# Kernel optimization log

Hardware: AMD Instinct MI355X
Metric: run time of the kernel (lower is better)

Reference implementation:

```python
import jax, jax.numpy as jnp
import numpy as np

B, N, DIM = 4, 2048, 1024
HEADS, DHEAD = 16, 64
INNER = HEADS * DHEAD  # 1024


def _sigma(t):
    # elu(x) + 1 feature map (strictly positive)
    return jax.nn.elu(t) + 1.0


def setup_inputs() -> dict:
    key = jax.random.key(0)
    k1, k2, k3, k4, k5 = jax.random.split(key, 5)
    x = jax.random.normal(k1, (B, N, DIM), dtype=jnp.float32)
    M = jax.random.normal(k2, (B, HEADS, DHEAD, DHEAD), dtype=jnp.float32)
    Z = jnp.ones((B, HEADS, DHEAD, 1), dtype=jnp.float32)
    W_qkv = jax.random.normal(k3, (DIM, 3 * INNER), dtype=jnp.float32) * (DIM ** -0.5)
    beta_lin = jnp.ones((1,), dtype=jnp.float32) * 4.6     # Linear_Attention.beta
    beta_gate = jax.random.normal(k4, (1, HEADS, 1, 1), dtype=jnp.float32)  # per-head gate
    return {"x": x, "M": M, "Z": Z, "W_qkv": W_qkv, "beta_lin": beta_lin, "beta_gate": beta_gate}


def reference(x, M, Z, W_qkv, beta_lin, beta_gate):
    b, n, _ = x.shape
    scale = DHEAD ** -0.5

    qkv = x @ W_qkv                                   # [b, n, 3*inner]
    q, k, v = jnp.split(qkv, 3, axis=-1)
    # b n (h d) -> b h n d
    to_heads = lambda t: t.reshape(b, n, HEADS, DHEAD).transpose(0, 2, 1, 3)
    q, k, v = to_heads(q), to_heads(k), to_heads(v)

    # ---- linear-attention compressive memory branch ----
    sq = _sigma(q)                                    # [b h n d]
    sk = _sigma(k)
    A_mem = jnp.einsum('bhnd,bhdv->bhnv', sq, M) / jnp.einsum('bhnd,bhdi->bhni', sq, Z)
    moment = jnp.einsum('bhnd,bhdv->bhnv', sk, M) / jnp.einsum('bhnd,bhdi->bhni', sk, Z)

    # EMA state update (training path)
    beta_m = jnp.clip(jax.nn.sigmoid(beta_lin), 0.9, 0.999)  # scalar in (0.9, 0.999)
    Z_new = beta_m * Z + jnp.sum(sk, axis=-2)[..., None]      # [b h d 1]
    M_new = beta_m * M + jnp.einsum('bhnd,bhnv->bhdv', sk, v - moment)

    # ---- standard dot-product attention branch ----
    dots = jnp.einsum('bhid,bhjd->bhij', q, k) * scale
    attn = jax.nn.softmax(dots, axis=-1)
    A_dot = jnp.einsum('bhij,bhjd->bhid', attn, v)

    # ---- learned per-head gate ----
    g = jax.nn.sigmoid(beta_gate)                     # [1 h 1 1]
    A = g * A_mem + (1.0 - g) * A_dot                 # [b h n d]
    A = A.transpose(0, 2, 1, 3).reshape(b, n, INNER)  # b h n d -> b n (h d)
    return (A, M_new, Z_new)
```

## Files before the change

### kernel.cpp

```cpp
#include <hip/hip_runtime.h>
#include <math.h>

#define B_ 4
#define N_ 2048
#define DIM_ 1024
#define H_ 16
#define D_ 64
#define INNER_ 1024
#define BH_ (B_*H_)

#define A_ELEMS  (B_*N_*INNER_)
#define M_ELEMS  (BH_*D_*D_)
#define Z_ELEMS  (BH_*D_)

#define SC_LOG2E 0.18033688011112042f

typedef __attribute__((ext_vector_type(8))) short short8;
typedef __attribute__((ext_vector_type(4))) float f32x4;
typedef __attribute__((ext_vector_type(4))) unsigned short us4;
typedef unsigned short u16;

__device__ __forceinline__ u16 f2bf(float f) {
    unsigned int u = __float_as_uint(f);
    u += 0x7fffu + ((u >> 16) & 1u);
    return (u16)(u >> 16);
}
__device__ __forceinline__ float bf2f(u16 s) {
    return __uint_as_float(((unsigned int)s) << 16);
}
__device__ __forceinline__ float sigma_f(float x) {
    return x > 0.f ? x + 1.f : __expf(x);
}
__device__ __forceinline__ short8 sig8(short8 in) {
    short8 out;
    u16* ip = (u16*)&in; u16* op = (u16*)&out;
    #pragma unroll
    for (int c = 0; c < 8; c++) op[c] = f2bf(sigma_f(bf2f(ip[c])));
    return out;
}

__global__ __launch_bounds__(256) void cvt_x(const float* __restrict__ x,
                                             u16* __restrict__ xb) {
    long i = ((long)blockIdx.x * 256 + threadIdx.x) * 4;
    float4 f = *(const float4*)&x[i];
    us4 o = {f2bf(f.x), f2bf(f.y), f2bf(f.z), f2bf(f.w)};
    *(us4*)&xb[i] = o;
}

__global__ __launch_bounds__(256) void cvt_w(const float* __restrict__ W,
                                             u16* __restrict__ Wt) {
    __shared__ u16 T[64 * 68];
    const int t  = threadIdx.x;
    const int n0 = blockIdx.x * 64, k0 = blockIdx.y * 64;
    #pragma unroll
    for (int i = 0; i < 4; i++) {
        int r  = (t >> 4) + i * 16;
        int c4 = (t & 15) * 4;
        float4 f = *(const float4*)&W[(long)(k0 + r) * 3072 + n0 + c4];
        T[(c4 + 0) * 68 + r] = f2bf(f.x);
        T[(c4 + 1) * 68 + r] = f2bf(f.y);
        T[(c4 + 2) * 68 + r] = f2bf(f.z);
        T[(c4 + 3) * 68 + r] = f2bf(f.w);
    }
    __syncthreads();
    #pragma unroll
    for (int i = 0; i < 4; i++) {
        int n  = (t >> 4) + i * 16;
        int k4 = (t & 15) * 4;
        us4 o;
        o.x = T[n * 68 + k4];     o.y = T[n * 68 + k4 + 1];
        o.z = T[n * 68 + k4 + 2]; o.w = T[n * 68 + k4 + 3];
        *(us4*)&Wt[(long)(n0 + n) * 1024 + k0 + k4] = o;
    }
}

__global__ __launch_bounds__(256) void qkv_mfma(
    const u16* __restrict__ xb, const u16* __restrict__ Wt,
    u16* __restrict__ q, u16* __restrict__ k, u16* __restrict__ v,
    u16* __restrict__ qs) {
    __shared__ u16 As[128 * 40];
    __shared__ u16 Bs[128 * 40];
    const int t = threadIdx.x, w = t >> 6, lane = t & 63;
    const int quad = lane >> 4, l16 = lane & 15;
    const int m0 = blockIdx.y * 128, j0 = blockIdx.x * 128;
    const int mw = (w >> 1) * 64, nw = (w & 1) * 64;

    f32x4 acc[4][4] = {};

    for (int k0 = 0; k0 < DIM_; k0 += 32) {
        __syncthreads();
        #pragma unroll
        for (int i = 0; i < 2; i++) {
            int r = (t >> 2) + i * 64, kg = (t & 3) * 8;
            *(short8*)&As[r * 40 + kg] =
                *(const short8*)&xb[(long)(m0 + r) * 1024 + k0 + kg];
            *(short8*)&Bs[r * 40 + kg] =
                *(const short8*)&Wt[(long)(j0 + r) * 1024 + k0 + kg];
        }
        __syncthreads();

        short8 af[4], bf[4];
        #pragma unroll
        for (int mt = 0; mt < 4; mt++)
            af[mt] = *(const short8*)&As[(mw + mt * 16 + l16) * 40 + quad * 8];
        #pragma unroll
        for (int nt = 0; nt < 4; nt++)
            bf[nt] = *(const short8*)&Bs[(nw + nt * 16 + l16) * 40 + quad * 8];
        #pragma unroll
        for (int mt = 0; mt < 4; mt++)
            #pragma unroll
            for (int nt = 0; nt < 4; nt++)
                acc[mt][nt] = __builtin_amdgcn_mfma_f32_16x16x32_bf16(
                    af[mt], bf[nt], acc[mt][nt], 0, 0, 0);
    }

    #pragma unroll
    for (int mt = 0; mt < 4; mt++) {
        #pragma unroll
        for (int r = 0; r < 4; r++) {
            int mm = m0 + mw + mt * 16 + quad * 4 + r;
            int b  = mm >> 11, n = mm & 2047;
            #pragma unroll
            for (int nt = 0; nt < 4; nt++) {
                int col   = j0 + nw + nt * 16 + l16;
                int which = col >> 10;
                int rem   = col & 1023;
                int h = rem >> 6, d = rem & 63;
                long idx = (((long)(b * H_ + h)) * N_ + n) * D_ + d;
                float a = acc[mt][nt][r];
                u16 val = f2bf(a);
                if (which == 0) {
                    q[idx]  = val;
                    qs[idx] = f2bf(a * SC_LOG2E);
                } else {
                    u16* dst = (which == 1) ? k : v;
                    dst[idx] = val;
                }
            }
        }
    }
}

__global__ __launch_bounds__(256) void vt_transpose(
    const u16* __restrict__ vb, u16* __restrict__ vT) {
    __shared__ u16 T[64 * 72];
    const int bh = blockIdx.y;
    const int n0 = blockIdx.x * 64;
    const int t  = threadIdx.x;
    const int jj = t >> 3, kg = (t & 7) * 8;
    #pragma unroll
    for (int i = 0; i < 2; i++) {
        int j = jj + i * 32;
        short8 vv = *(const short8*)&vb[(((long)bh * N_ + n0 + j) << 6) + kg];
        u16* vp = (u16*)&vv;
        int jc = j ^ kg;
        #pragma unroll
        for (int c = 0; c < 8; c++) T[(kg + c) * 72 + jc] = vp[c];
    }
    __syncthreads();
    const int d = t >> 2, sg = (t & 3) * 16, xr = d & 56;
    short8 a0 = *(const short8*)&T[d * 72 + (sg ^ xr)];
    short8 a1 = *(const short8*)&T[d * 72 + ((sg + 8) ^ xr)];
    u16* dst = vT + ((long)bh * 64 + d) * 2048 + n0 + sg;
    *(short8*)dst       = a0;
    *(short8*)(dst + 8) = a1;
}

__global__ __launch_bounds__(256) void init_mz(
    const float* __restrict__ M, const float* __restrict__ Z,
    const float* __restrict__ beta_lin,
    float* __restrict__ outM, float* __restrict__ outZ) {
    float beta = 1.f / (1.f + __expf(-beta_lin[0]));
    beta = fminf(fmaxf(beta, 0.9f), 0.999f);
    int i = blockIdx.x * 256 + threadIdx.x;
    if (i < M_ELEMS) outM[i] = beta * M[i];
    if (i < Z_ELEMS) outZ[i] = beta * Z[i];
}

__global__ __launch_bounds__(256) void linear_mfma(
    const u16* __restrict__ qg, const u16* __restrict__ kg_,
    const u16* __restrict__ vTg, const float* __restrict__ Mg,
    const float* __restrict__ Zg, const float* __restrict__ beta_gate,
    float* __restrict__ outA, float* __restrict__ outM, float* __restrict__ outZ) {
    __shared__ u16 MTz[80 * 72];
    __shared__ u16 sqsh[64 * 72];
    __shared__ u16 sksh[64 * 72];
    __shared__ u16 skT[64 * 72];
    __shared__ u16 vT[64 * 72];
    __shared__ u16 vmT[80 * 72];
    __shared__ float dks[64];

    const int bh = blockIdx.y, b = bh >> 4, h = bh & 15;
    const int t = threadIdx.x, w = t >> 6, lane = t & 63;
    const int quad = lane >> 4, l16 = lane & 15;
    const long bhN = (long)bh * N_;

    #pragma unroll
    for (int i = 0; i < 4; i++) {
        int d  = (t >> 4) + i * 16;
        int c4 = (t & 15) * 4;
        float4 f = *(const float4*)&Mg[bh * 4096 + d * 64 + c4];
        MTz[(c4 + 0) * 72 + d] = f2bf(f.x);
        MTz[(c4 + 1) * 72 + d] = f2bf(f.y);
        MTz[(c4 + 2) * 72 + d] = f2bf(f.z);
        MTz[(c4 + 3) * 72 + d] = f2bf(f.w);
    }
    if (t < 64) {
        MTz[64 * 72 + t] = f2bf(Zg[bh * 64 + t]);
        vmT[64 * 72 + t] = f2bf(1.0f);
    }
    for (int e = t; e < 15 * 72; e += 256) {
        MTz[65 * 72 + e] = 0;
        vmT[65 * 72 + e] = 0;
    }
    if (t >= 64 && t < 72) { MTz[64 * 72 + t] = 0; vmT[64 * 72 + t] = 0; }

    const float g = 1.f / (1.f + __expf(-beta_gate[h]));

    f32x4 macc[5] = {};

    const int jj = t >> 3;
    const int kgp = (t & 7) * 8;
    const int srow = t >> 2;
    const int sg   = (t & 3) * 16;

    for (int c0 = 0; c0 < 256; c0 += 64) {
        const int n0c = blockIdx.x * 256 + c0;
        __syncthreads();

        #pragma unroll
        for (int i = 0; i < 2; i++) {
            int j = jj + i * 32;
            long gb = ((bhN + n0c + j) << 6) + kgp;
            short8 q8 = sig8(*(const short8*)&qg[gb]);
            short8 k8 = sig8(*(const short8*)&kg_[gb]);
            *(short8*)&sqsh[j * 72 + kgp] = q8;
            *(short8*)&sksh[j * 72 + kgp] = k8;
            u16* kp = (u16*)&k8;
            int jc = j ^ kgp;
            #pragma unroll
            for (int c = 0; c < 8; c++) skT[(kgp + c) * 72 + jc] = kp[c];
        }
        {
            const u16* vp = vTg + ((long)bh * 64 + srow) * 2048 + n0c + sg;
            *(short8*)&vT[srow * 72 + sg]     = *(const short8*)vp;
            *(short8*)&vT[srow * 72 + sg + 8] = *(const short8*)(vp + 8);
        }
        __syncthreads();

        {
            short8 a0 = *(const short8*)&sqsh[(w * 16 + l16) * 72 + quad * 8];
            short8 a1 = *(const short8*)&sqsh[(w * 16 + l16) * 72 + 32 + quad * 8];
            f32x4 am[5];
            #pragma unroll
            for (int ct = 0; ct < 5; ct++) {
                short8 b0 = *(const short8*)&MTz[(ct * 16 + l16) * 72 + quad * 8];
                short8 b1 = *(const short8*)&MTz[(ct * 16 + l16) * 72 + 32 + quad * 8];
                f32x4 acc = {};
                acc = __builtin_amdgcn_mfma_f32_16x16x32_bf16(a0, b0, acc, 0, 0, 0);
                acc = __builtin_amdgcn_mfma_f32_16x16x32_bf16(a1, b1, acc, 0, 0, 0);
                am[ct] = acc;
            }
            #pragma unroll
            for (int r = 0; r < 4; r++) {
                float dq  = __shfl(am[4][r], lane & 48, 64);
                float inv = __builtin_amdgcn_rcpf(dq);
                int n = n0c + w * 16 + quad * 4 + r;
                long row = ((long)(b * N_ + n)) * INNER_ + h * 64;
                #pragma unroll
                for (int ct = 0; ct < 4; ct++)
                    outA[row + ct * 16 + l16] = g * am[ct][r] * inv;
            }
        }

        f32x4 mt_[4];
        {
            short8 a0 = *(const short8*)&MTz[(w * 16 + l16) * 72 + quad * 8];
            short8 a1 = *(const short8*)&MTz[(w * 16 + l16) * 72 + 32 + quad * 8];
            #pragma unroll
            for (int ct = 0; ct < 4; ct++) {
                short8 b0 = *(const short8*)&sksh[(ct * 16 + l16) * 72 + quad * 8];
                short8 b1 = *(const short8*)&sksh[(ct * 16 + l16) * 72 + 32 + quad * 8];
                f32x4 acc = {};
                acc = __builtin_amdgcn_mfma_f32_16x16x32_bf16(a0, b0, acc, 0, 0, 0);
                acc = __builtin_amdgcn_mfma_f32_16x16x32_bf16(a1, b1, acc, 0, 0, 0);
                mt_[ct] = acc;
            }
            short8 z0 = *(const short8*)&MTz[(64 + l16) * 72 + quad * 8];
            short8 z1 = *(const short8*)&MTz[(64 + l16) * 72 + 32 + quad * 8];
            short8 b0 = *(const short8*)&sksh[(w * 16 + l16) * 72 + quad * 8];
            short8 b1 = *(const short8*)&sksh[(w * 16 + l16) * 72 + 32 + quad * 8];
            f32x4 acc = {};
            acc = __builtin_amdgcn_mfma_f32_16x16x32_bf16(z0, b0, acc, 0, 0, 0);
            acc = __builtin_amdgcn_mfma_f32_16x16x32_bf16(z1, b1, acc, 0, 0, 0);
            if (quad == 0) dks[w * 16 + l16] = __builtin_amdgcn_rcpf(acc[0]);
        }
        __syncthreads();

        #pragma unroll
        for (int ct = 0; ct < 4; ct++) {
            float invdk = dks[ct * 16 + l16];
            #pragma unroll
            for (int r = 0; r < 4; r++) {
                int vd = w * 16 + quad * 4 + r;
                float vv = bf2f(vT[vd * 72 + ct * 16 + l16]);
                vmT[vd * 72 + ct * 16 + l16] = f2bf(vv - mt_[ct][r] * invdk);
            }
        }
        __syncthreads();

        {
            int drow = w * 16 + l16, xr = drow & 56;
            short8 a0 = *(const short8*)&skT[drow * 72 + ((quad * 8) ^ xr)];
            short8 a1 = *(const short8*)&skT[drow * 72 + ((32 + quad * 8) ^ xr)];
            #pragma unroll
            for (int ct = 0; ct < 5; ct++) {
                short8 b0 = *(const short8*)&vmT[(ct * 16 + l16) * 72 + quad * 8];
                short8 b1 = *(const short8*)&vmT[(ct * 16 + l16) * 72 + 32 + quad * 8];
                macc[ct] = __builtin_amdgcn_mfma_f32_16x16x32_bf16(a0, b0, macc[ct], 0, 0, 0);
                macc[ct] = __builtin_amdgcn_mfma_f32_16x16x32_bf16(a1, b1, macc[ct], 0, 0, 0);
            }
        }
    }

    #pragma unroll
    for (int ct = 0; ct < 4; ct++)
        #pragma unroll
        for (int r = 0; r < 4; r++) {
            int d = w * 16 + quad * 4 + r;
            atomicAdd(&outM[bh * 4096 + d * 64 + ct * 16 + l16], macc[ct][r]);
        }
    if (l16 == 0)
        #pragma unroll
        for (int r = 0; r < 4; r++)
            atomicAdd(&outZ[bh * 64 + w * 16 + quad * 4 + r], macc[4][r]);
}

__global__ __launch_bounds__(256) void flash_mfma(
    const u16* __restrict__ qsb, const u16* __restrict__ kb,
    const u16* __restrict__ vTg, const float* __restrict__ beta_gate,
    float* __restrict__ outA) {
    __shared__ u16 Ks[64 * 72];
    __shared__ u16 Vt[64 * 72];
    __shared__ u16 Ps[4][32 * 72];

    const int bh = blockIdx.y, b = bh >> 4, h = bh & 15;
    const int n0 = blockIdx.x * 128;
    const int t = threadIdx.x, w = t >> 6, lane = t & 63;
    const int quad = lane >> 4, l16 = lane & 15;
    const long bhN = (long)bh * N_;

    const int srow = t >> 2;
    const int sg   = (t & 3) * 16;
    const u16* kbase  = kb + (bhN << 6);
    const u16* vtbase = vTg + (long)bh * 64 * 2048;

    short8 qf[2][2];
    #pragma unroll
    for (int mi = 0; mi < 2; mi++) {
        long qrow = bhN + n0 + w * 32 + mi * 16 + l16;
        qf[mi][0] = *(const short8*)&qsb[(qrow << 6) + quad * 8];
        qf[mi][1] = *(const short8*)&qsb[(qrow << 6) + 32 + quad * 8];
    }

    const short8 onesf = {0x3F80, 0x3F80, 0x3F80, 0x3F80,
                          0x3F80, 0x3F80, 0x3F80, 0x3F80};

    short8 kr0, kr1, vr0, vr1;
    {
        const u16* kp = kbase + ((long)srow << 6) + sg;
        kr0 = *(const short8*)kp;
        kr1 = *(const short8*)(kp + 8);
        const u16* vp = vtbase + (long)srow * 2048 + sg;
        vr0 = *(const short8*)vp;
        vr1 = *(const short8*)(vp + 8);
    }

    f32x4 of[2][4] = {};
    f32x4 ol[2] = {};

    for (int j0 = 0; j0 < N_; j0 += 64) {
        __syncthreads();
        *(short8*)&Ks[srow * 72 + sg]     = kr0;
        *(short8*)&Ks[srow * 72 + sg + 8] = kr1;
        *(short8*)&Vt[srow * 72 + sg]     = vr0;
        *(short8*)&Vt[srow * 72 + sg + 8] = vr1;
        __syncthreads();

        if (j0 + 64 < N_) {
            const u16* kp = kbase + ((long)(j0 + 64 + srow) << 6) + sg;
            kr0 = *(const short8*)kp;
            kr1 = *(const short8*)(kp + 8);
            const u16* vp = vtbase + (long)srow * 2048 + j0 + 64 + sg;
            vr0 = *(const short8*)vp;
            vr1 = *(const short8*)(vp + 8);
        }

        #pragma unroll
        for (int kt = 0; kt < 4; kt++) {
            short8 kf0 = *(const short8*)&Ks[(kt * 16 + l16) * 72 + quad * 8];
            short8 kf1 = *(const short8*)&Ks[(kt * 16 + l16) * 72 + 32 + quad * 8];
            #pragma unroll
            for (int mi = 0; mi < 2; mi++) {
                f32x4 st = {};
                st = __builtin_amdgcn_mfma_f32_16x16x32_bf16(kf0, qf[mi][0], st, 0, 0, 0);
                st = __builtin_amdgcn_mfma_f32_16x16x32_bf16(kf1, qf[mi][1], st, 0, 0, 0);
                float p0 = __builtin_amdgcn_exp2f(st[0]);
                float p1 = __builtin_amdgcn_exp2f(st[1]);
                float p2 = __builtin_amdgcn_exp2f(st[2]);
                float p3 = __builtin_amdgcn_exp2f(st[3]);
                uint2 pk;
                pk.x = __builtin_amdgcn_perm(__float_as_uint(p1), __float_as_uint(p0),
                                             0x07060302u);
                pk.y = __builtin_amdgcn_perm(__float_as_uint(p3), __float_as_uint(p2),
                                             0x07060302u);
                *(uint2*)&Ps[w][(mi * 16 + l16) * 72 + kt * 16 + quad * 4] = pk;
            }
        }

        #pragma unroll
        for (int s = 0; s < 2; s++) {
            short8 af0 = *(const short8*)&Ps[w][(l16) * 72 + s * 32 + quad * 8];
            short8 af1 = *(const short8*)&Ps[w][(16 + l16) * 72 + s * 32 + quad * 8];
            ol[0] = __builtin_amdgcn_mfma_f32_16x16x32_bf16(af0, onesf, ol[0], 0, 0, 0);
            ol[1] = __builtin_amdgcn_mfma_f32_16x16x32_bf16(af1, onesf, ol[1], 0, 0, 0);
            #pragma unroll
            for (int nt = 0; nt < 4; nt++) {
                short8 vf = *(const short8*)&Vt[(nt * 16 + l16) * 72 + s * 32 + quad * 8];
                of[0][nt] = __builtin_amdgcn_mfma_f32_16x16x32_bf16(af0, vf, of[0][nt], 0, 0, 0);
                of[1][nt] = __builtin_amdgcn_mfma_f32_16x16x32_bf16(af1, vf, of[1][nt], 0, 0, 0);
            }
        }
    }

    const float g  = 1.f / (1.f + __expf(-beta_gate[h]));
    const float gi = 1.f - g;
    #pragma unroll
    for (int mi = 0; mi < 2; mi++) {
        #pragma unroll
        for (int r = 0; r < 4; r++) {
            float sc = gi / ol[mi][r];
            int n = n0 + w * 32 + mi * 16 + quad * 4 + r;
            #pragma unroll
            for (int nt = 0; nt < 4; nt++) {
                long idx = ((long)(b * N_ + n)) * INNER_ + h * 64 + nt * 16 + l16;
                outA[idx] += sc * of[mi][nt][r];
            }
        }
    }
}

extern "C" void kernel_launch(void* const* d_in, const int* in_sizes, int n_in,
                              void* d_out, int out_size, void* d_ws, size_t ws_size,
                              hipStream_t stream) {
    const float* x         = (const float*)d_in[0];
    const float* M         = (const float*)d_in[1];
    const float* Z         = (const float*)d_in[2];
    const float* W         = (const float*)d_in[3];
    const float* beta_lin  = (const float*)d_in[4];
    const float* beta_gate = (const float*)d_in[5];

    float* out  = (float*)d_out;
    float* outA = out;
    float* outM = out + A_ELEMS;
    float* outZ = out + A_ELEMS + M_ELEMS;

    u16* xb = (u16*)d_ws;
    u16* Wt = xb + (size_t)8192 * 1024;
    u16* qb = Wt + (size_t)3072 * 1024;
    u16* kb = qb + (size_t)BH_ * N_ * D_;
    u16* vb = kb + (size_t)BH_ * N_ * D_;
    u16* vt = vb + (size_t)BH_ * N_ * D_;
    u16* qs = vt + (size_t)BH_ * N_ * D_;

    cvt_x<<<dim3(A_ELEMS / 1024), 256, 0, stream>>>(x, xb);
    cvt_w<<<dim3(48, 16), 256, 0, stream>>>(W, Wt);
    qkv_mfma<<<dim3(24, 64), 256, 0, stream>>>(xb, Wt, qb, kb, vb, qs);
    vt_transpose<<<dim3(N_ / 64, BH_), 256, 0, stream>>>(vb, vt);
    init_mz<<<dim3((M_ELEMS + 255) / 256), 256, 0, stream>>>(M, Z, beta_lin, outM, outZ);
    linear_mfma<<<dim3(8, BH_), 256, 0, stream>>>(qb, kb, vt, M, Z, beta_gate,
                                                  outA, outM, outZ);
    flash_mfma<<<dim3(N_ / 128, BH_), 256, 0, stream>>>(qs, kb, vt, beta_gate, outA);
}
```

Before: 301.2 us.

## Keep softmax probabilities in registers by permuting K rows in shared memory

Removes the per-wave Ps shared-memory round trip for the attention probabilities. K rows are stored in shared memory under a permuted row order, so the QK^T MFMA output layout lines up directly with the A-operand layout of the PV MFMA. The exponentiated scores are packed straight into a bf16 register fragment. This cuts LDS writes and reads and the dependency on them per tile, at the cost of a non-obvious row permutation whose correctness depends on the exact MFMA lane mapping.

Measured after the change: 294.9 us. 1.02x faster.

```diff
diff --git a/kernel.cpp b/kernel.cpp
--- a/kernel.cpp
+++ b/kernel.cpp
@@ -342,7 +342,6 @@
     float* __restrict__ outA) {
     __shared__ u16 Ks[64 * 72];
     __shared__ u16 Vt[64 * 72];
-    __shared__ u16 Ps[4][32 * 72];
 
     const int bh = blockIdx.y, b = bh >> 4, h = bh & 15;
     const int n0 = blockIdx.x * 128;
@@ -352,6 +351,9 @@
 
     const int srow = t >> 2;
     const int sg   = (t & 3) * 16;
+    const int jloc = srow & 31;
+    const int krow = (srow & 32) + ((jloc & 4) << 2) + ((jloc >> 3) << 2) + (jloc & 3);
+
     const u16* kbase  = kb + (bhN << 6);
     const u16* vtbase = vTg + (long)bh * 64 * 2048;
 
@@ -381,8 +383,8 @@
 
     for (int j0 = 0; j0 < N_; j0 += 64) {
         __syncthreads();
-        *(short8*)&Ks[srow * 72 + sg]     = kr0;
-        *(short8*)&Ks[srow * 72 + sg + 8] = kr1;
+        *(short8*)&Ks[krow * 72 + sg]     = kr0;
+        *(short8*)&Ks[krow * 72 + sg + 8] = kr1;
         *(short8*)&Vt[srow * 72 + sg]     = vr0;
         *(short8*)&Vt[srow * 72 + sg + 8] = vr1;
         __syncthreads();
@@ -397,38 +399,47 @@
         }
 
         #pragma unroll
-        for (int kt = 0; kt < 4; kt++) {
-            short8 kf0 = *(const short8*)&Ks[(kt * 16 + l16) * 72 + quad * 8];
-            short8 kf1 = *(const short8*)&Ks[(kt * 16 + l16) * 72 + 32 + quad * 8];
+        for (int g = 0; g < 2; g++) {
+            const int rb = g * 32;
+            short8 kA0 = *(const short8*)&Ks[(rb + l16) * 72 + quad * 8];
+            short8 kA1 = *(const short8*)&Ks[(rb + l16) * 72 + 32 + quad * 8];
+            short8 kB0 = *(const short8*)&Ks[(rb + 16 + l16) * 72 + quad * 8];
+            short8 kB1 = *(const short8*)&Ks[(rb + 16 + l16) * 72 + 32 + quad * 8];
+            short8 vf[4];
+            #pragma unroll
+            for (int nt = 0; nt < 4; nt++)
+                vf[nt] = *(const short8*)&Vt[(nt * 16 + l16) * 72 + rb + quad * 8];
+
             #pragma unroll
             for (int mi = 0; mi < 2; mi++) {
-                f32x4 st = {};
-                st = __builtin_amdgcn_mfma_f32_16x16x32_bf16(kf0, qf[mi][0], st, 0, 0, 0);
-                st = __builtin_amdgcn_mfma_f32_16x16x32_bf16(kf1, qf[mi][1], st, 0, 0, 0);
-                float p0 = __builtin_amdgcn_exp2f(st[0]);
-                float p1 = __builtin_amdgcn_exp2f(st[1]);
-                float p2 = __builtin_amdgcn_exp2f(st[2]);
-                float p3 = __builtin_amdgcn_exp2f(st[3]);
-                uint2 pk;
-                pk.x = __builtin_amdgcn_perm(__float_as_uint(p1), __float_as_uint(p0),
-                                             0x07060302u);
-                pk.y = __builtin_amdgcn_perm(__float_as_uint(p3), __float_as_uint(p2),
-                                             0x07060302u);
-                *(uint2*)&Ps[w][(mi * 16 + l16) * 72 + kt * 16 + quad * 4] = pk;
-            }
-        }
-
-        #pragma unroll
-        for (int s = 0; s < 2; s++) {
-            short8 af0 = *(const short8*)&Ps[w][(l16) * 72 + s * 32 + quad * 8];
-            short8 af1 = *(const short8*)&Ps[w][(16 + l16) * 72 + s * 32 + quad * 8];
-            ol[0] = __builtin_amdgcn_mfma_f32_16x16x32_bf16(af0, onesf, ol[0], 0, 0, 0);
-            ol[1] = __builtin_amdgcn_mfma_f32_16x16x32_bf16(af1, onesf, ol[1], 0, 0, 0);
-            #pragma unroll
-            for (int nt = 0; nt < 4; nt++) {
-                short8 vf = *(const short8*)&Vt[(nt * 16 + l16) * 72 + s * 32 + quad * 8];
-                of[0][nt] = __builtin_amdgcn_mfma_f32_16x16x32_bf16(af0, vf, of[0][nt], 0, 0, 0);
-                of[1][nt] = __builtin_amdgcn_mfma_f32_16x16x32_bf16(af1, vf, of[1][nt], 0, 0, 0);
+                f32x4 st0 = {}, st1 = {};
+                st0 = __builtin_amdgcn_mfma_f32_16x16x32_bf16(kA0, qf[mi][0], st0, 0, 0, 0);
+                st0 = __builtin_amdgcn_mfma_f32_16x16x32_bf16(kA1, qf[mi][1], st0, 0, 0, 0);
+                st1 = __builtin_amdgcn_mfma_f32_16x16x32_bf16(kB0, qf[mi][0], st1, 0, 0, 0);
+                st1 = __builtin_amdgcn_mfma_f32_16x16x32_bf16(kB1, qf[mi][1], st1, 0, 0, 0);
+                float p0 = __builtin_amdgcn_exp2f(st0[0]);
+                float p1 = __builtin_amdgcn_exp2f(st0[1]);
+                float p2 = __builtin_amdgcn_exp2f(st0[2]);
+                float p3 = __builtin_amdgcn_exp2f(st0[3]);
+                float p4 = __builtin_amdgcn_exp2f(st1[0]);
+                float p5 = __builtin_amdgcn_exp2f(st1[1]);
+                float p6 = __builtin_amdgcn_exp2f(st1[2]);
+                float p7 = __builtin_amdgcn_exp2f(st1[3]);
+                short8 af;
+                unsigned int* au = (unsigned int*)&af;
+                au[0] = __builtin_amdgcn_perm(__float_as_uint(p1), __float_as_uint(p0),
+                                              0x07060302u);
+                au[1] = __builtin_amdgcn_perm(__float_as_uint(p3), __float_as_uint(p2),
+                                              0x07060302u);
+                au[2] = __builtin_amdgcn_perm(__float_as_uint(p5), __float_as_uint(p4),
+                                              0x07060302u);
+                au[3] = __builtin_amdgcn_perm(__float_as_uint(p7), __float_as_uint(p6),
+                                              0x07060302u);
+                ol[mi] = __builtin_amdgcn_mfma_f32_16x16x32_bf16(af, onesf, ol[mi], 0, 0, 0);
+                #pragma unroll
+                for (int nt = 0; nt < 4; nt++)
+                    of[mi][nt] = __builtin_amdgcn_mfma_f32_16x16x32_bf16(
+                        af, vf[nt], of[mi][nt], 0, 0, 0);
             }
         }
     }
```
